# Kernel tuning notes

Measured on AMD Instinct MI355X. Metric: run time of the kernel, lower is better.

The kernel has to match this reference:

```python
import jax, jax.numpy as jnp
import numpy as np

# dims
N, E, B, T = 1024, 8192, 4, 8          # nodes, edges, batch, time steps
IN, HID, H, NCLASS = 64, 64, 4, 7      # in_dim, nhidden, heads, nclass
K = N - NCLASS + 1                     # output-head conv width
NEG, EPS = 0.2, 1e-5


def setup_inputs() -> dict:
    key = jax.random.key(0)
    ks = jax.random.split(key, 24)
    p = lambda i, shape: jax.random.normal(ks[i], shape, jnp.float32) * 0.05
    inputs = jax.random.normal(ks[0], (B, IN, T, N), jnp.float32)
    src = jax.random.randint(ks[1], (E,), 0, N, jnp.int32)
    dst = jnp.repeat(jnp.arange(N, dtype=jnp.int32), E // N)  # every node has in-degree 8
    return {
        "inputs": inputs, "src": src, "dst": dst,
        "W0": p(2, (H * HID, IN)), "al0": p(3, (H, HID)), "ar0": p(4, (H, HID)),
        "W1": p(5, (H * HID, H * HID)), "al1": p(6, (H, HID)), "ar1": p(7, (H, HID)),
        "W2": p(8, (H * 1, H * HID)), "al2": p(9, (H, 1)), "ar2": p(10, (H, 1)),
        "Wres2": p(11, (H * 1, H * HID)),
        # Outputlayer
        "tc1_w": p(12, (H, H, T)), "tc1_b": p(13, (H,)),
        "ln1_g": jnp.ones((N, H), jnp.float32), "ln1_b": jnp.zeros((N, H), jnp.float32),
        "tc2_w": p(14, (1, H)), "tc2_b": p(15, (1,)),
        "ln2_g": jnp.ones((N, 1), jnp.float32), "ln2_b": jnp.zeros((N, 1), jnp.float32),
        "fc_w": p(16, (K,)), "fc_b": p(17, (1,)),
    }


def _gat_conv(h, src, dst, W, al, ar, res=None, act=None):
    # h: (N,B,T,F) -> feat: (N,B,T,H,D)
    heads, d = al.shape
    feat = (h @ W.T).reshape(N, B, T, heads, d)
    el = jnp.einsum('nbthd,hd->nbth', feat, al)
    er = jnp.einsum('nbthd,hd->nbth', feat, ar)
    e = jax.nn.leaky_relu(el[src] + er[dst], NEG)           # (E,B,T,H)
    emax = jax.ops.segment_max(e, dst, num_segments=N)
    ex = jnp.exp(e - emax[dst])
    den = jax.ops.segment_sum(ex, dst, num_segments=N)
    a = ex / den[dst]                                        # edge softmax over incoming edges
    out = jax.ops.segment_sum(feat[src] * a[..., None], dst, num_segments=N)  # (N,B,T,H,D)
    if res is not None:
        out = out + res
    if act is not None:
        out = act(out)
    return out


def reference(inputs, src, dst,
              W0, al0, ar0, W1, al1, ar1, W2, al2, ar2, Wres2,
              tc1_w, tc1_b, ln1_g, ln1_b, tc2_w, tc2_b, ln2_g, ln2_b, fc_w, fc_b):
    # (B,IN,T,N) -> (N,B,T,IN) : transpose(0,3).transpose(1,3)
    h = jnp.transpose(inputs.astype(jnp.float32), (3, 0, 2, 1))
    h1 = _gat_conv(h, src, dst, W0, al0, ar0, act=jax.nn.elu).reshape(N, B, T, H * HID)
    h2 = _gat_conv(h1, src, dst, W1, al1, ar1,
                   res=h1.reshape(N, B, T, H, HID), act=jax.nn.elu).reshape(N, B, T, H * HID)
    res2 = (h2 @ Wres2.T).reshape(N, B, T, H, 1)
    o = _gat_conv(h2, src, dst, W2, al2, ar2, res=res2)      # (N,B,T,H,1)
    # transpose(1,3).transpose(0,3).squeeze(-1) -> (B,H,T,N)
    x = jnp.transpose(o[..., 0], (1, 3, 2, 0))

    # Outputlayer
    # tconv1: Conv2d(H->H, kernel (T,1)) collapses time -> (B,H,N)
    x1 = jnp.einsum('oht,bhtn->bon', tc1_w, x) + tc1_b[None, :, None]
    # ln1: LayerNorm over (N,H) of (B,1,N,H)
    z = jnp.transpose(x1, (0, 2, 1))                          # (B,N,H)
    mu = z.mean(axis=(1, 2), keepdims=True)
    var = z.var(axis=(1, 2), keepdims=True)
    z = (z - mu) / jnp.sqrt(var + EPS) * ln1_g + ln1_b
    x1 = jnp.transpose(z, (0, 2, 1))                          # (B,H,N)
    # tconv2: 1x1 conv H->1 -> (B,1,N)
    x2 = jnp.einsum('oh,bhn->bon', tc2_w, x1) + tc2_b[None, :, None]
    # ln2: LayerNorm over (N,1)
    mu = x2.mean(axis=2, keepdims=True)
    var = x2.var(axis=2, keepdims=True)
    x2 = (x2 - mu) / jnp.sqrt(var + EPS) * ln2_g[:, 0] + ln2_b[:, 0]
    # fc: Conv2d(1->1, kernel (1,K)) sliding over nodes -> (B,NCLASS)
    xc = x2[:, :, None, :]                                    # (B,1,1,N) NCHW
    w = fc_w[None, None, None, :]                             # (1,1,1,K) OIHW
    out = jax.lax.conv_general_dilated(xc, w, (1, 1), 'VALID') + fc_b[None, :, None, None]
    return out[:, 0, 0, :]                                    # (B, NCLASS)
```

## Files before the change

kernel.cpp:

```cpp
#include <hip/hip_runtime.h>
#include <math.h>

#define NEGS 0.2f
#define EPSF 1e-5f

typedef short s16x8 __attribute__((ext_vector_type(8)));
typedef float f32x4 __attribute__((ext_vector_type(4)));

__device__ __forceinline__ float b2f(unsigned short u) {
  union { unsigned int i; float f; } v; v.i = ((unsigned int)u) << 16; return v.f;
}
__device__ __forceinline__ unsigned short f2b(float f) {
  union { float f; unsigned int i; } v; v.f = f;
  unsigned int x = v.i;
  return (unsigned short)((x + 0x7fffu + ((x >> 16) & 1u)) >> 16);
}
__device__ __forceinline__ float elu_neg(float x) { return __expf(x) - 1.f; }

__device__ __forceinline__ void gbar(int* slot, int sub) {
  __syncthreads();
  if (threadIdx.x == 0) {
    int old = __hip_atomic_fetch_add(slot + sub*16, 1, __ATOMIC_RELAXED, __HIP_MEMORY_SCOPE_AGENT);
    if (old == 31) {
      int om = __hip_atomic_fetch_add(slot + 64, 1, __ATOMIC_RELAXED, __HIP_MEMORY_SCOPE_AGENT);
      if (om == 3)
        __hip_atomic_store(slot + 96, 1, __ATOMIC_RELEASE, __HIP_MEMORY_SCOPE_AGENT);
    }
    int it = 0;
    while (__hip_atomic_load(slot + 96, __ATOMIC_RELAXED, __HIP_MEMORY_SCOPE_AGENT) == 0) {
      __builtin_amdgcn_s_sleep(2);
      if (++it > (1 << 22)) break;
    }
  }
  __syncthreads();
}

__global__ __launch_bounds__(256, 4) void k_mega(
    const float* __restrict__ inp, const int* __restrict__ src,
    const float* __restrict__ W0, const float* __restrict__ al0, const float* __restrict__ ar0,
    const float* __restrict__ W1, const float* __restrict__ al1, const float* __restrict__ ar1,
    const float* __restrict__ W2, const float* __restrict__ al2, const float* __restrict__ ar2,
    const float* __restrict__ Wr2, const float* __restrict__ tc1w,
    unsigned short* __restrict__ W1bX, unsigned short* __restrict__ feat0,
    unsigned short* __restrict__ feat1,
    float* __restrict__ el0, float* __restrict__ er0,
    float* __restrict__ el1, float* __restrict__ er1,
    float* __restrict__ feat2, float* __restrict__ res2,
    float* __restrict__ x1, int* bar)
{
  __shared__ __align__(16) char pool[22528];
  int (*ssm)[8] = (int(*)[8])(pool + 21248);
  const int tid = threadIdx.x;
  const int bid = blockIdx.x;
  const int g     = bid & 7;
  const int bt    = g*4 + ((bid >> 3) & 3);
  const int nBase = (bid >> 5) * 32;
  const int sub   = (bid >> 3) & 3;
  const int b = bt >> 3, t = bt & 7;
  const int w = tid >> 6, lane = tid & 63, n16 = lane & 15, q = lane >> 4;

  s16x8 h1r[2][2];

  {
    unsigned short (*At)[72] = (unsigned short(*)[72])pool;
    unsigned short *Lb = (unsigned short*)(pool + 4608);
    ((int*)ssm)[tid] = src[nBase*8 + tid];
    s16x8 bf[2][4];
    #pragma unroll
    for (int kc = 0; kc < 2; ++kc)
      #pragma unroll
      for (int ct = 0; ct < 4; ++ct) {
        const float* p = &W0[(size_t)((w*4 + ct)*16 + n16)*64 + kc*32 + q*8];
        float4 wa = *(const float4*)p;
        float4 wb = *(const float4*)(p + 4);
        s16x8 o;
        o[0]=(short)f2b(wa.x); o[1]=(short)f2b(wa.y); o[2]=(short)f2b(wa.z); o[3]=(short)f2b(wa.w);
        o[4]=(short)f2b(wb.x); o[5]=(short)f2b(wb.y); o[6]=(short)f2b(wb.z); o[7]=(short)f2b(wb.w);
        bf[kc][ct] = o;
      }
    {
      const int nn = tid & 7, cg = tid >> 3;
      #pragma unroll
      for (int c2 = 0; c2 < 2; ++c2) {
        const int ch = cg + c2*32;
        float4 v = *(const float4*)&inp[((size_t)(b*64 + ch)*8 + t)*1024 + nBase + nn*4];
        At[nn*4 + 0][ch] = f2b(v.x);
        At[nn*4 + 1][ch] = f2b(v.y);
        At[nn*4 + 2][ch] = f2b(v.z);
        At[nn*4 + 3][ch] = f2b(v.w);
      }
    }
    __syncthreads();
    f32x4 acc[2][4];
    #pragma unroll
    for (int rt = 0; rt < 2; ++rt)
      #pragma unroll
      for (int ct = 0; ct < 4; ++ct) acc[rt][ct] = (f32x4){0.f,0.f,0.f,0.f};
    #pragma unroll
    for (int kc = 0; kc < 2; ++kc) {
      s16x8 af[2];
      #pragma unroll
      for (int rt = 0; rt < 2; ++rt)
        af[rt] = *(const s16x8*)&At[rt*16 + n16][kc*32 + q*8];
      #pragma unroll
      for (int rt = 0; rt < 2; ++rt)
        #pragma unroll
        for (int ct = 0; ct < 4; ++ct)
          acc[rt][ct] = __builtin_amdgcn_mfma_f32_16x16x32_bf16(af[rt], bf[kc][ct], acc[rt][ct], 0, 0, 0);
    }
    float alv[4], arv[4];
    #pragma unroll
    for (int ct = 0; ct < 4; ++ct) {
      alv[ct] = al0[w*64 + ct*16 + n16];
      arv[ct] = ar0[w*64 + ct*16 + n16];
    }
    #pragma unroll
    for (int rt = 0; rt < 2; ++rt) {
      #pragma unroll
      for (int reg = 0; reg < 4; ++reg) {
        float pl = acc[rt][0][reg]*alv[0] + acc[rt][1][reg]*alv[1]
                 + acc[rt][2][reg]*alv[2] + acc[rt][3][reg]*alv[3];
        float pr = acc[rt][0][reg]*arv[0] + acc[rt][1][reg]*arv[1]
                 + acc[rt][2][reg]*arv[2] + acc[rt][3][reg]*arv[3];
        #pragma unroll
        for (int o = 1; o < 16; o <<= 1) { pl += __shfl_xor(pl, o); pr += __shfl_xor(pr, o); }
        if (n16 == 0) {
          int r = (nBase + rt*16 + q*4 + reg)*32 + bt;
          el0[r*4 + w] = pl;
          er0[r*4 + w] = pr;
        }
      }
    }
    #pragma unroll
    for (int rt = 0; rt < 2; ++rt)
      #pragma unroll
      for (int ct = 0; ct < 4; ++ct)
        #pragma unroll
        for (int reg = 0; reg < 4; ++reg)
          Lb[(rt*16 + q*4 + reg)*256 + w*64 + ct*16 + n16] = f2b(acc[rt][ct][reg]);
    __syncthreads();
    #pragma unroll
    for (int i = 0; i < 4; ++i) {
      int u = tid + i*256;
      int m = u >> 5, off = (u & 31) * 8;
      *(s16x8*)&feat0[(size_t)((nBase + m)*32 + bt)*256 + off] = *(const s16x8*)&Lb[m*256 + off];
    }
    if (tid < 128) {
      const int j = ((bid >> 3) << 9) + tid*4;
      float4 w4 = *(const float4*)&W1[j];
      ushort4 o4; o4.x=f2b(w4.x); o4.y=f2b(w4.y); o4.z=f2b(w4.z); o4.w=f2b(w4.w);
      *(ushort4*)&W1bX[(size_t)g*65536 + j] = o4;
    }
  }
  gbar(bar + (0*8 + g)*128, sub);

  {
    float (*wsm)[8][4] = (float(*)[8][4])pool;
    unsigned short *smbuf = (unsigned short*)(pool + 4096);
    unsigned short (*At)[264] = (unsigned short(*)[264])smbuf;
    unsigned short *Lb = smbuf;
    const int hw2 = tid >> 5, l5 = tid & 31;
    const int c0 = l5 * 8, hh = l5 >> 3;
    s16x8 vA[8], vB[8];
    #pragma unroll
    for (int j = 0; j < 8; ++j) {
      vA[j] = *(const s16x8*)&feat0[(size_t)(ssm[hw2    ][j]*32 + bt)*256 + c0];
      vB[j] = *(const s16x8*)&feat0[(size_t)(ssm[hw2 + 8][j]*32 + bt)*256 + c0];
    }
    if (tid < 128) {
      const int nl = tid >> 2, h = tid & 3;
      const int rn = (nBase + nl)*32 + bt;
      const float erv = er0[rn*4 + h];
      float e[8]; float mx = -1e30f;
      #pragma unroll
      for (int j = 0; j < 8; ++j) {
        float v = el0[(ssm[nl][j]*32 + bt)*4 + h] + erv;
        v = v >= 0.f ? v : NEGS * v;
        e[j] = v; mx = fmaxf(mx, v);
      }
      float den = 0.f;
      #pragma unroll
      for (int j = 0; j < 8; ++j) { e[j] = __expf(e[j] - mx); den += e[j]; }
      const float inv = 1.f / den;
      #pragma unroll
      for (int j = 0; j < 8; ++j) wsm[nl][j][h] = e[j] * inv;
    }
    __syncthreads();
    #pragma unroll
    for (int p2 = 0; p2 < 2; ++p2) {
      const int nlA = p2*16 + hw2, nlB = nlA + 8;
      if (p2 == 1) {
        #pragma unroll
        for (int j = 0; j < 8; ++j) {
          vA[j] = *(const s16x8*)&feat0[(size_t)(ssm[nlA][j]*32 + bt)*256 + c0];
          vB[j] = *(const s16x8*)&feat0[(size_t)(ssm[nlB][j]*32 + bt)*256 + c0];
        }
      }
      asm volatile("" ::: "memory");
      float aA[8] = {0,0,0,0,0,0,0,0}, aB[8] = {0,0,0,0,0,0,0,0};
      #pragma unroll
      for (int j = 0; j < 8; ++j) {
        const float wA = wsm[nlA][j][hh], wB = wsm[nlB][j][hh];
        #pragma unroll
        for (int i = 0; i < 8; ++i) {
          aA[i] = fmaf(wA, b2f((unsigned short)vA[j][i]), aA[i]);
          aB[i] = fmaf(wB, b2f((unsigned short)vB[j][i]), aB[i]);
        }
      }
      s16x8 oA, oB;
      #pragma unroll
      for (int i = 0; i < 8; ++i) {
        float xA = aA[i] > 0.f ? aA[i] : elu_neg(aA[i]);
        float xB = aB[i] > 0.f ? aB[i] : elu_neg(aB[i]);
        oA[i] = (short)f2b(xA); oB[i] = (short)f2b(xB);
      }
      *(s16x8*)&At[nlA][c0] = oA;
      *(s16x8*)&At[nlB][c0] = oB;
      h1r[p2][0] = oA;
      h1r[p2][1] = oB;
    }
    __syncthreads();
    f32x4 acc[2][4];
    #pragma unroll
    for (int rt = 0; rt < 2; ++rt)
      #pragma unroll
      for (int ct = 0; ct < 4; ++ct) acc[rt][ct] = (f32x4){0.f,0.f,0.f,0.f};
    const unsigned short* W1g = W1bX + (size_t)g*65536;
    #pragma unroll
    for (int kc = 0; kc < 8; ++kc) {
      s16x8 af[2], bfr[4];
      #pragma unroll
      for (int rt = 0; rt < 2; ++rt)
        af[rt] = *(const s16x8*)&At[rt*16 + n16][kc*32 + q*8];
      #pragma unroll
      for (int ct = 0; ct < 4; ++ct)
        bfr[ct] = *(const s16x8*)&W1g[(size_t)((w*4 + ct)*16 + n16)*256 + kc*32 + q*8];
      #pragma unroll
      for (int rt = 0; rt < 2; ++rt)
        #pragma unroll
        for (int ct = 0; ct < 4; ++ct)
          acc[rt][ct] = __builtin_amdgcn_mfma_f32_16x16x32_bf16(af[rt], bfr[ct], acc[rt][ct], 0, 0, 0);
    }
    float alv[4], arv[4];
    #pragma unroll
    for (int ct = 0; ct < 4; ++ct) {
      alv[ct] = al1[w*64 + ct*16 + n16];
      arv[ct] = ar1[w*64 + ct*16 + n16];
    }
    #pragma unroll
    for (int rt = 0; rt < 2; ++rt) {
      #pragma unroll
      for (int reg = 0; reg < 4; ++reg) {
        float pl = acc[rt][0][reg]*alv[0] + acc[rt][1][reg]*alv[1]
                 + acc[rt][2][reg]*alv[2] + acc[rt][3][reg]*alv[3];
        float pr = acc[rt][0][reg]*arv[0] + acc[rt][1][reg]*arv[1]
                 + acc[rt][2][reg]*arv[2] + acc[rt][3][reg]*arv[3];
        #pragma unroll
        for (int o = 1; o < 16; o <<= 1) { pl += __shfl_xor(pl, o); pr += __shfl_xor(pr, o); }
        if (n16 == 0) {
          int r = (nBase + rt*16 + q*4 + reg)*32 + bt;
          el1[r*4 + w] = pl;
          er1[r*4 + w] = pr;
        }
      }
    }
    __syncthreads();
    #pragma unroll
    for (int rt = 0; rt < 2; ++rt)
      #pragma unroll
      for (int ct = 0; ct < 4; ++ct)
        #pragma unroll
        for (int reg = 0; reg < 4; ++reg)
          Lb[(rt*16 + q*4 + reg)*256 + w*64 + ct*16 + n16] = f2b(acc[rt][ct][reg]);
    __syncthreads();
    #pragma unroll
    for (int i = 0; i < 4; ++i) {
      int u = tid + i*256;
      int row = u >> 5, off = (u & 31) * 8;
      *(s16x8*)&feat1[(size_t)((nBase + row)*32 + bt)*256 + off] = *(const s16x8*)&Lb[row*256 + off];
    }
  }
  gbar(bar + (1*8 + g)*128, sub);

  {
    float (*wsm)[8][4] = (float(*)[8][4])pool;
    float (*Wp)[256]   = (float(*)[256])(pool + 4096);
    const int hw2 = tid >> 5, l5 = tid & 31;
    const int c0 = l5 * 8, hh = l5 >> 3;
    s16x8 vA[8], vB[8];
    #pragma unroll
    for (int j = 0; j < 8; ++j) {
      vA[j] = *(const s16x8*)&feat1[(size_t)(ssm[hw2    ][j]*32 + bt)*256 + c0];
      vB[j] = *(const s16x8*)&feat1[(size_t)(ssm[hw2 + 8][j]*32 + bt)*256 + c0];
    }
    ((float4*)Wp)[tid]       = ((const float4*)W2)[tid & 255];
    ((float4*)Wp)[256 + tid] = ((const float4*)Wr2)[tid & 255];
    if (tid < 128) {
      const int nl = tid >> 2, h = tid & 3;
      const int rn = (nBase + nl)*32 + bt;
      const float erv = er1[rn*4 + h];
      float e[8]; float mx = -1e30f;
      #pragma unroll
      for (int j = 0; j < 8; ++j) {
        float v = el1[(ssm[nl][j]*32 + bt)*4 + h] + erv;
        v = v >= 0.f ? v : NEGS * v;
        e[j] = v; mx = fmaxf(mx, v);
      }
      float den = 0.f;
      #pragma unroll
      for (int j = 0; j < 8; ++j) { e[j] = __expf(e[j] - mx); den += e[j]; }
      const float inv = 1.f / den;
      #pragma unroll
      for (int j = 0; j < 8; ++j) wsm[nl][j][h] = e[j] * inv;
    }
    __syncthreads();
    #pragma unroll
    for (int p2 = 0; p2 < 2; ++p2) {
      const int nlA = p2*16 + hw2, nlB = nlA + 8;
      const int rnA = (nBase + nlA)*32 + bt, rnB = (nBase + nlB)*32 + bt;
      if (p2 == 1) {
        #pragma unroll
        for (int j = 0; j < 8; ++j) {
          vA[j] = *(const s16x8*)&feat1[(size_t)(ssm[nlA][j]*32 + bt)*256 + c0];
          vB[j] = *(const s16x8*)&feat1[(size_t)(ssm[nlB][j]*32 + bt)*256 + c0];
        }
      }
      asm volatile("" ::: "memory");
      const s16x8 rrA = h1r[p2][0], rrB = h1r[p2][1];
      float aA[8] = {0,0,0,0,0,0,0,0}, aB[8] = {0,0,0,0,0,0,0,0};
      #pragma unroll
      for (int j = 0; j < 8; ++j) {
        const float wA = wsm[nlA][j][hh], wB = wsm[nlB][j][hh];
        #pragma unroll
        for (int i = 0; i < 8; ++i) {
          aA[i] = fmaf(wA, b2f((unsigned short)vA[j][i]), aA[i]);
          aB[i] = fmaf(wB, b2f((unsigned short)vB[j][i]), aB[i]);
        }
      }
      #pragma unroll
      for (int i = 0; i < 8; ++i) {
        float xA = aA[i] + b2f((unsigned short)rrA[i]);
        float xB = aB[i] + b2f((unsigned short)rrB[i]);
        aA[i] = xA > 0.f ? xA : elu_neg(xA);
        aB[i] = xB > 0.f ? xB : elu_neg(xB);
      }
      #pragma unroll
      for (int o = 0; o < 8; ++o) {
        float4 wa = *(const float4*)&Wp[o][c0];
        float4 wb = *(const float4*)&Wp[o][c0 + 4];
        float pA = aA[0]*wa.x + aA[1]*wa.y + aA[2]*wa.z + aA[3]*wa.w
                 + aA[4]*wb.x + aA[5]*wb.y + aA[6]*wb.z + aA[7]*wb.w;
        float pB = aB[0]*wa.x + aB[1]*wa.y + aB[2]*wa.z + aB[3]*wa.w
                 + aB[4]*wb.x + aB[5]*wb.y + aB[6]*wb.z + aB[7]*wb.w;
        #pragma unroll
        for (int off = 1; off < 32; off <<= 1) {
          pA += __shfl_xor(pA, off);
          pB += __shfl_xor(pB, off);
        }
        if (l5 == 0) {
          if (o < 4) { feat2[rnA*4 + o] = pA; feat2[rnB*4 + o] = pB; }
          else       { res2[rnA*4 + (o-4)] = pA; res2[rnB*4 + (o-4)] = pB; }
        }
      }
    }
  }
  gbar(bar + (2*8 + g)*128, sub);

  if (tid < 128) {
    const int nl = tid >> 2, h = tid & 3;
    const int n = nBase + nl;
    const int rn = n*32 + bt;
    const float av = al2[h], rv = ar2[h];
    const float erv = feat2[rn*4 + h] * rv;
    float f[8], e[8]; float m = -1e30f;
    #pragma unroll
    for (int j = 0; j < 8; ++j) {
      f[j] = feat2[(ssm[nl][j]*32 + bt)*4 + h];
      float v = f[j]*av + erv;
      v = v >= 0.f ? v : NEGS * v;
      e[j] = v; m = fmaxf(m, v);
    }
    float den = 0.f, num = 0.f;
    #pragma unroll
    for (int j = 0; j < 8; ++j) { float ex = __expf(e[j]-m); den += ex; num = fmaf(ex, f[j], num); }
    const float os = num/den + res2[rn*4 + h];
    float po[4];
    #pragma unroll
    for (int o = 0; o < 4; ++o) po[o] = tc1w[(o*4 + h)*8 + t] * os;
    #pragma unroll
    for (int off = 1; off < 4; off <<= 1)
      #pragma unroll
      for (int o = 0; o < 4; ++o) po[o] += __shfl_xor(po[o], off);
    float v = (h==0) ? po[0] : (h==1) ? po[1] : (h==2) ? po[2] : po[3];
    atomicAdd(&x1[(b*4 + h)*1024 + n], v);
  }
}

__global__ __launch_bounds__(256) void k_fin(
    const float* __restrict__ x1g, const float* __restrict__ tc1b,
    const float* __restrict__ ln1g, const float* __restrict__ ln1b,
    const float* __restrict__ tc2w, const float* __restrict__ tc2b,
    const float* __restrict__ ln2g, const float* __restrict__ ln2b,
    const float* __restrict__ fcw, const float* __restrict__ fcb,
    float* __restrict__ out)
{
  __shared__ __align__(16) float x1s[4][1024];
  __shared__ float x2s[1024];
  __shared__ float redA[4], redB[4];
  __shared__ float redC[4][7];
  const int bb = blockIdx.x, tid = threadIdx.x;
  const int wv = tid >> 6, lane = tid & 63;
  float s = 0.f, qq = 0.f;
  #pragma unroll
  for (int i = 0; i < 4; ++i) {
    const int n = tid + i*256;
    #pragma unroll
    for (int o = 0; o < 4; ++o) {
      float a = x1g[(bb*4 + o)*1024 + n] + tc1b[o];
      x1s[o][n] = a; s += a; qq += a*a;
    }
  }
  #pragma unroll
  for (int o = 32; o > 0; o >>= 1) { s += __shfl_down(s, o); qq += __shfl_down(qq, o); }
  if (lane == 0) { redA[wv] = s; redB[wv] = qq; }
  __syncthreads();
  const float S = redA[0]+redA[1]+redA[2]+redA[3];
  const float Q = redB[0]+redB[1]+redB[2]+redB[3];
  const float mu  = S * (1.f/4096.f);
  const float var = Q * (1.f/4096.f) - mu*mu;
  const float inv = rsqrtf(var + EPSF);
  const float tb = tc2b[0];
  const float r0 = tc2w[0], r1 = tc2w[1], r2 = tc2w[2], r3 = tc2w[3];
  float accv[4]; float s2 = 0.f, q2 = 0.f;
  #pragma unroll
  for (int i = 0; i < 4; ++i) {
    const int n = tid + i*256;
    float4 g4 = *(const float4*)&ln1g[n*4];
    float4 b4 = *(const float4*)&ln1b[n*4];
    float a = tb;
    a = fmaf(r0, (x1s[0][n]-mu)*inv*g4.x + b4.x, a);
    a = fmaf(r1, (x1s[1][n]-mu)*inv*g4.y + b4.y, a);
    a = fmaf(r2, (x1s[2][n]-mu)*inv*g4.z + b4.z, a);
    a = fmaf(r3, (x1s[3][n]-mu)*inv*g4.w + b4.w, a);
    accv[i] = a; s2 += a; q2 += a*a;
  }
  __syncthreads();
  #pragma unroll
  for (int o = 32; o > 0; o >>= 1) { s2 += __shfl_down(s2, o); q2 += __shfl_down(q2, o); }
  if (lane == 0) { redA[wv] = s2; redB[wv] = q2; }
  __syncthreads();
  const float S2 = redA[0]+redA[1]+redA[2]+redA[3];
  const float Q2 = redB[0]+redB[1]+redB[2]+redB[3];
  const float mu2  = S2 * (1.f/1024.f);
  const float inv2 = rsqrtf(Q2 * (1.f/1024.f) - mu2*mu2 + EPSF);
  #pragma unroll
  for (int i = 0; i < 4; ++i) {
    const int n = tid + i*256;
    x2s[n] = (accv[i] - mu2) * inv2 * ln2g[n] + ln2b[n];
  }
  __syncthreads();
  float pc[7] = {0.f,0.f,0.f,0.f,0.f,0.f,0.f};
  for (int k = tid; k < 1018; k += 256) {
    const float fw = fcw[k];
    #pragma unroll
    for (int c = 0; c < 7; ++c) pc[c] = fmaf(x2s[k + c], fw, pc[c]);
  }
  #pragma unroll
  for (int o = 32; o > 0; o >>= 1)
    #pragma unroll
    for (int c = 0; c < 7; ++c) pc[c] += __shfl_down(pc[c], o);
  if (lane == 0) {
    #pragma unroll
    for (int c = 0; c < 7; ++c) redC[wv][c] = pc[c];
  }
  __syncthreads();
  if (tid < 7)
    out[bb*7 + tid] = redC[0][tid] + redC[1][tid] + redC[2][tid] + redC[3][tid] + fcb[0];
}

extern "C" void kernel_launch(void* const* d_in, const int* in_sizes, int n_in,
                              void* d_out, int out_size, void* d_ws, size_t ws_size,
                              hipStream_t stream)
{
  const float* inp  = (const float*)d_in[0];
  const int*   src  = (const int*)  d_in[1];
  const float* W0   = (const float*)d_in[3];
  const float* al0  = (const float*)d_in[4];
  const float* ar0  = (const float*)d_in[5];
  const float* W1   = (const float*)d_in[6];
  const float* al1  = (const float*)d_in[7];
  const float* ar1  = (const float*)d_in[8];
  const float* W2   = (const float*)d_in[9];
  const float* al2  = (const float*)d_in[10];
  const float* ar2  = (const float*)d_in[11];
  const float* Wr2  = (const float*)d_in[12];
  const float* tc1w = (const float*)d_in[13];
  const float* tc1b = (const float*)d_in[14];
  const float* ln1g = (const float*)d_in[15];
  const float* ln1b = (const float*)d_in[16];
  const float* tc2w = (const float*)d_in[17];
  const float* tc2b = (const float*)d_in[18];
  const float* ln2g = (const float*)d_in[19];
  const float* ln2b = (const float*)d_in[20];
  const float* fcw  = (const float*)d_in[21];
  const float* fcb  = (const float*)d_in[22];
  float* out = (float*)d_out;

  unsigned short* W1bX   = (unsigned short*)d_ws;
  unsigned short* featb0 = W1bX   + 524288;
  unsigned short* featb1 = featb0 + 8388608;
  float* el0   = (float*)(featb1 + 8388608);
  float* er0   = el0   + 131072;
  float* el1   = er0   + 131072;
  float* er1   = el1   + 131072;
  float* feat2 = er1   + 131072;
  float* res2  = feat2 + 131072;
  float* x1    = res2  + 131072;
  int*   bar   = (int*)(x1 + 16384);

  hipMemsetAsync(x1, 0, 16384*4 + 12288, stream);
  k_mega<<<dim3(1024), dim3(256), 0, stream>>>(inp, src, W0, al0, ar0, W1, al1, ar1,
                                               W2, al2, ar2, Wr2, tc1w,
                                               W1bX, featb0, featb1,
                                               el0, er0, el1, er1, feat2, res2, x1, bar);
  k_fin<<<dim3(4), dim3(256), 0, stream>>>(x1, tc1b, ln1g, ln1b, tc2w, tc2b,
                                           ln2g, ln2b, fcw, fcb, out);
}
```

Baseline: 178.7 us.

## Compute layer-2 projection with bf16 MFMA and keep residual in shared memory

The final GAT layer's 256->8 projection (W2 and Wres2) moves from per-thread FP32 dot products with 32-lane shuffle reductions onto a bf16 MFMA 16x16x32 pass. The ELU outputs are staged in LDS as bf16 and the weights are converted to bf16 in LDS first. The residual and the node's own feat2 values now stay in shared memory for the last stage, so the global res2 buffer and its round-trip are gone. In exchange, LDS use per block grows, the projection runs at bf16 precision, and only two waves do the MFMA work.

```diff
diff --git a/kernel.cpp b/kernel.cpp
--- a/kernel.cpp
+++ b/kernel.cpp
@@ -45,11 +45,13 @@
     unsigned short* __restrict__ feat1,
     float* __restrict__ el0, float* __restrict__ er0,
     float* __restrict__ el1, float* __restrict__ er1,
-    float* __restrict__ feat2, float* __restrict__ res2,
+    float* __restrict__ feat2,
     float* __restrict__ x1, int* bar)
 {
-  __shared__ __align__(16) char pool[22528];
-  int (*ssm)[8] = (int(*)[8])(pool + 21248);
+  __shared__ __align__(16) char pool[27392];
+  int   (*ssm)[8]  = (int(*)[8])(pool + 26368);
+  float (*res_s)[4] = (float(*)[4])(pool + 25344);
+  float (*f2_s)[4]  = (float(*)[4])(pool + 25856);
   const int tid = threadIdx.x;
   const int bid = blockIdx.x;
   const int g     = bid & 7;
@@ -284,7 +286,8 @@
 
   {
     float (*wsm)[8][4] = (float(*)[8][4])pool;
-    float (*Wp)[256]   = (float(*)[256])(pool + 4096);
+    unsigned short (*At2)[264] = (unsigned short(*)[264])(pool + 4096);
+    unsigned short (*Wcb)[272] = (unsigned short(*)[272])(pool + 20992);
     const int hw2 = tid >> 5, l5 = tid & 31;
     const int c0 = l5 * 8, hh = l5 >> 3;
     s16x8 vA[8], vB[8];
@@ -293,8 +296,16 @@
       vA[j] = *(const s16x8*)&feat1[(size_t)(ssm[hw2    ][j]*32 + bt)*256 + c0];
       vB[j] = *(const s16x8*)&feat1[(size_t)(ssm[hw2 + 8][j]*32 + bt)*256 + c0];
     }
-    ((float4*)Wp)[tid]       = ((const float4*)W2)[tid & 255];
-    ((float4*)Wp)[256 + tid] = ((const float4*)Wr2)[tid & 255];
+    {
+      const int r = tid >> 5, c8 = (tid & 31) * 8;
+      const float* sw = (r < 4) ? &W2[r*256 + c8] : &Wr2[(r-4)*256 + c8];
+      float4 aa = *(const float4*)sw;
+      float4 bb = *(const float4*)(sw + 4);
+      s16x8 o;
+      o[0]=(short)f2b(aa.x); o[1]=(short)f2b(aa.y); o[2]=(short)f2b(aa.z); o[3]=(short)f2b(aa.w);
+      o[4]=(short)f2b(bb.x); o[5]=(short)f2b(bb.y); o[6]=(short)f2b(bb.z); o[7]=(short)f2b(bb.w);
+      *(s16x8*)&Wcb[r][c8] = o;
+    }
     if (tid < 128) {
       const int nl = tid >> 2, h = tid & 3;
       const int rn = (nBase + nl)*32 + bt;
@@ -317,7 +328,6 @@
     #pragma unroll
     for (int p2 = 0; p2 < 2; ++p2) {
       const int nlA = p2*16 + hw2, nlB = nlA + 8;
-      const int rnA = (nBase + nlA)*32 + bt, rnB = (nBase + nlB)*32 + bt;
       if (p2 == 1) {
         #pragma unroll
         for (int j = 0; j < 8; ++j) {
@@ -337,29 +347,38 @@
           aB[i] = fmaf(wB, b2f((unsigned short)vB[j][i]), aB[i]);
         }
       }
+      s16x8 oA, oB;
       #pragma unroll
       for (int i = 0; i < 8; ++i) {
         float xA = aA[i] + b2f((unsigned short)rrA[i]);
         float xB = aB[i] + b2f((unsigned short)rrB[i]);
-        aA[i] = xA > 0.f ? xA : elu_neg(xA);
-        aB[i] = xB > 0.f ? xB : elu_neg(xB);
-      }
-      #pragma unroll
-      for (int o = 0; o < 8; ++o) {
-        float4 wa = *(const float4*)&Wp[o][c0];
-        float4 wb = *(const float4*)&Wp[o][c0 + 4];
-        float pA = aA[0]*wa.x + aA[1]*wa.y + aA[2]*wa.z + aA[3]*wa.w
-                 + aA[4]*wb.x + aA[5]*wb.y + aA[6]*wb.z + aA[7]*wb.w;
-        float pB = aB[0]*wa.x + aB[1]*wa.y + aB[2]*wa.z + aB[3]*wa.w
-                 + aB[4]*wb.x + aB[5]*wb.y + aB[6]*wb.z + aB[7]*wb.w;
-        #pragma unroll
-        for (int off = 1; off < 32; off <<= 1) {
-          pA += __shfl_xor(pA, off);
-          pB += __shfl_xor(pB, off);
-        }
-        if (l5 == 0) {
-          if (o < 4) { feat2[rnA*4 + o] = pA; feat2[rnB*4 + o] = pB; }
-          else       { res2[rnA*4 + (o-4)] = pA; res2[rnB*4 + (o-4)] = pB; }
+        xA = xA > 0.f ? xA : elu_neg(xA);
+        xB = xB > 0.f ? xB : elu_neg(xB);
+        oA[i] = (short)f2b(xA); oB[i] = (short)f2b(xB);
+      }
+      *(s16x8*)&At2[nlA][c0] = oA;
+      *(s16x8*)&At2[nlB][c0] = oB;
+    }
+    __syncthreads();
+    if (w < 2) {
+      const int rt = w;
+      f32x4 acc = (f32x4){0.f,0.f,0.f,0.f};
+      #pragma unroll
+      for (int kc = 0; kc < 8; ++kc) {
+        s16x8 af = *(const s16x8*)&At2[rt*16 + n16][kc*32 + q*8];
+        s16x8 bfr = (s16x8){0,0,0,0,0,0,0,0};
+        if (n16 < 8) bfr = *(const s16x8*)&Wcb[n16][kc*32 + q*8];
+        acc = __builtin_amdgcn_mfma_f32_16x16x32_bf16(af, bfr, acc, 0, 0, 0);
+      }
+      #pragma unroll
+      for (int reg = 0; reg < 4; ++reg) {
+        const int nl = rt*16 + q*4 + reg;
+        const float v = acc[reg];
+        if (n16 < 4) {
+          feat2[((size_t)(nBase + nl)*32 + bt)*4 + n16] = v;
+          f2_s[nl][n16] = v;
+        } else if (n16 < 8) {
+          res_s[nl][n16 - 4] = v;
         }
       }
     }
@@ -369,9 +388,8 @@
   if (tid < 128) {
     const int nl = tid >> 2, h = tid & 3;
     const int n = nBase + nl;
-    const int rn = n*32 + bt;
     const float av = al2[h], rv = ar2[h];
-    const float erv = feat2[rn*4 + h] * rv;
+    const float erv = f2_s[nl][h] * rv;
     float f[8], e[8]; float m = -1e30f;
     #pragma unroll
     for (int j = 0; j < 8; ++j) {
@@ -383,7 +401,7 @@
     float den = 0.f, num = 0.f;
     #pragma unroll
     for (int j = 0; j < 8; ++j) { float ex = __expf(e[j]-m); den += ex; num = fmaf(ex, f[j], num); }
-    const float os = num/den + res2[rn*4 + h];
+    const float os = num/den + res_s[nl][h];
     float po[4];
     #pragma unroll
     for (int o = 0; o < 4; ++o) po[o] = tc1w[(o*4 + h)*8 + t] * os;
@@ -514,15 +532,14 @@
   float* el1   = er0   + 131072;
   float* er1   = el1   + 131072;
   float* feat2 = er1   + 131072;
-  float* res2  = feat2 + 131072;
-  float* x1    = res2  + 131072;
+  float* x1    = feat2 + 131072;
   int*   bar   = (int*)(x1 + 16384);
 
   hipMemsetAsync(x1, 0, 16384*4 + 12288, stream);
   k_mega<<<dim3(1024), dim3(256), 0, stream>>>(inp, src, W0, al0, ar0, W1, al1, ar1,
                                                W2, al2, ar2, Wr2, tc1w,
                                                W1bX, featb0, featb1,
-                                               el0, er0, el1, er1, feat2, res2, x1, bar);
+                                               el0, er0, el1, er1, feat2, x1, bar);
   k_fin<<<dim3(4), dim3(256), 0, stream>>>(x1, tc1b, ln1g, ln1b, tc2w, tc2b,
                                            ln2g, ln2b, fcw, fcb, out);
 }
```

Measured after the change: 171.2 us. 4.2% less time.
